# Optimization experiments

Measured on AMD Instinct MI355X. Metric: run time of the kernel, lower is better.

## Reference

```python
import jax, jax.numpy as jnp
import numpy as np

B, TAU, D, DX, DZ, H = 512, 4, 5, 256, 16, 64
M = D * DZ
COEFF_KL = 1.0
LOG2PI = float(np.log(2.0 * np.pi))


def setup_inputs() -> dict:
    ks = jax.random.split(jax.random.key(0), 12)
    s = 0.05
    return {
        "x": jax.random.normal(ks[0], (B, TAU, D, DX), jnp.float32),
        "y": jax.random.normal(ks[1], (B, D, DX), jnp.float32),
        "mask_param": jnp.full((TAU, M, M), 5.0, jnp.float32),
        "w_enc": ((0.9 * jax.random.uniform(ks[2], (D, DZ, DX)) + 0.1) / DX).astype(jnp.float32),
        "w_dec": ((0.9 * jax.random.uniform(ks[3], (D, DX, DZ)) + 0.1) / DZ).astype(jnp.float32),
        "enc_W0": jax.random.normal(ks[4], (DZ, DX, H), jnp.float32) * s,
        "enc_b0": jnp.zeros((DZ, H), jnp.float32),
        "enc_W1": jax.random.normal(ks[5], (DZ, H), jnp.float32) * s,
        "enc_b1": jnp.zeros((DZ,), jnp.float32),
        "dec_W0": jax.random.normal(ks[6], (DX, DZ, H), jnp.float32) * s,
        "dec_b0": jnp.zeros((DX, H), jnp.float32),
        "dec_W1": jax.random.normal(ks[7], (DX, H), jnp.float32) * s,
        "dec_b1": jnp.zeros((DX,), jnp.float32),
        "t_W0": jax.random.normal(ks[8], (M, TAU * M, H), jnp.float32) * s,
        "t_b0": jnp.zeros((M, H), jnp.float32),
        "t_W1": jax.random.normal(ks[9], (M, H), jnp.float32) * s,
        "t_b1": jnp.zeros((M,), jnp.float32),
        "logvar_enc": jnp.full((D,), -1.0, jnp.float32),
        "logvar_dec": jnp.full((D,), -1.0, jnp.float32),
        "t_logvar": jnp.full((D, DZ), -4.0, jnp.float32),
    }


def _encode(x, w_enc, W0, b0, W1, b1):
    # x: (..., D, DX) -> mu: (..., D, DZ); d_z tiny MLPs gated by mixing weights
    masked = w_enc * x[..., None, :]  # (..., D, DZ, DX)
    h = jax.nn.leaky_relu(jnp.einsum('...ijx,jxh->...ijh', masked, W0) + b0)
    return jnp.einsum('...ijh,jh->...ij', h, W1) + b1


def _forward(x, y, mask_param, w_enc, w_dec, enc_W0, enc_b0, enc_W1, enc_b1,
             dec_W0, dec_b0, dec_W1, dec_b1, t_W0, t_b0, t_W1, t_b1,
             logvar_enc, logvar_dec, t_logvar):
    b = x.shape[0]
    k_adj, k_ep, k_et = jax.random.split(jax.random.key(42), 3)
    # gumbel-sigmoid soft adjacency sample (temperature 1, drawhard=False)
    u = jax.random.uniform(k_adj, (b, TAU, M, M), minval=1e-6, maxval=1.0 - 1e-6)
    adj = jax.nn.sigmoid(mask_param + jnp.log(u) - jnp.log1p(-u))  # (b,TAU,M,M)
    # encoder q(z|x): reparameterized gaussian, per-feature logvar
    q_std = jnp.exp(0.5 * logvar_enc)[:, None]                     # (D,1)
    mu_past = _encode(x, w_enc, enc_W0, enc_b0, enc_W1, enc_b1)    # (b,TAU,D,DZ)
    z_past = mu_past + q_std * jax.random.normal(k_ep, mu_past.shape, jnp.float32)
    mu_t = _encode(y, w_enc, enc_W0, enc_b0, enc_W1, enc_b1)       # (b,D,DZ)
    z_t = mu_t + q_std * jax.random.normal(k_et, mu_t.shape, jnp.float32)
    # transition p(z_t|z_<t): per-node MLP on adjacency-gated past latents
    zp = z_past.reshape(b, TAU, M)
    gated = adj * zp[:, :, None, :]                                # (b,TAU,node,src)
    gated = gated.transpose(0, 2, 1, 3).reshape(b, M, TAU * M)
    ht = jax.nn.leaky_relu(jnp.einsum('bmi,mih->bmh', gated, t_W0) + t_b0)
    pz_mu = (jnp.einsum('bmh,mh->bm', ht, t_W1) + t_b1).reshape(b, D, DZ)
    pz_std = jnp.exp(0.5 * t_logvar)                               # (D,DZ)
    # decoder p(x|z): d_x tiny MLPs on mixing-mask-gated latents
    masked_z = w_dec * z_t[:, :, None, :]                          # (b,D,DX,DZ)
    hd = jax.nn.leaky_relu(jnp.einsum('bijz,jzh->bijh', masked_z, dec_W0) + dec_b0)
    px_mu = jnp.einsum('bijh,jh->bij', hd, dec_W1) + dec_b1        # (b,D,DX)
    px_std = jnp.exp(0.5 * logvar_dec)[:, None]                    # (D,1)
    # ELBO: gaussian recon log-lik + analytic gaussian KL(q || p_transition)
    recon = -0.5 * ((y - px_mu) / px_std) ** 2 - jnp.log(px_std) - 0.5 * LOG2PI
    recon = recon.sum(axis=(1, 2)).mean()
    kl = (jnp.log(pz_std) - 0.5 * logvar_enc[:, None]
          + (q_std ** 2 + (mu_t - pz_mu) ** 2) / (2.0 * pz_std ** 2) - 0.5)
    kl = kl.sum(axis=(1, 2)).mean()
    return -(recon - COEFF_KL * kl)


def reference(x, y, mask_param, w_enc, w_dec, enc_W0, enc_b0, enc_W1, enc_b1,
              dec_W0, dec_b0, dec_W1, dec_b1, t_W0, t_b0, t_W1, t_b1,
              logvar_enc, logvar_dec, t_logvar):
    return _forward(x, y, mask_param, w_enc, w_dec, enc_W0, enc_b0, enc_W1, enc_b1,
                    dec_W0, dec_b0, dec_W1, dec_b1, t_W0, t_b0, t_W1, t_b1,
                    logvar_enc, logvar_dec, t_logvar)
```

## Files before the change

kernel.cpp:

```cpp
#include <hip/hip_runtime.h>
#include <cstdint>

constexpr int NB = 512, NTAU = 4, ND = 5, NDX = 256, NDZ = 16, NH = 64;
constexpr int NM  = ND * NDZ;
constexpr int NTM = NTAU * NM;
constexpr int NSAMP = NB * NTAU + NB;
constexpr float LOG2PI_F = 1.8378770664093453f;

typedef __attribute__((ext_vector_type(8))) short bf16x8;
typedef __attribute__((ext_vector_type(4))) float f32x4;

__device__ __forceinline__ unsigned long long mix64(unsigned long long z) {
  z += 0x9E3779B97F4A7C15ull;
  z = (z ^ (z >> 30)) * 0xBF58476D1CE4E5B9ull;
  z = (z ^ (z >> 27)) * 0x94D049BB133111EBull;
  return z ^ (z >> 31);
}
__device__ __forceinline__ float u01f(unsigned long long h) {
  return ((float)(unsigned)(h >> 40) + 0.5f) * (1.0f / 16777216.0f);
}
__device__ __forceinline__ float rng_normal(unsigned long long salt, unsigned long long idx) {
  float u1 = u01f(mix64(salt + 2ull * idx));
  float u2 = u01f(mix64(salt + 2ull * idx + 1ull));
  float r = sqrtf(-2.0f * logf(u1));
  return r * cosf(6.283185307179586f * u2);
}
constexpr unsigned long long SALT_ADJ = 0x1000000000000ull;
constexpr unsigned long long SALT_EP  = 0x2000000000000ull;
constexpr unsigned long long SALT_ET  = 0x3000000000000ull;

__device__ __forceinline__ short f2bf(float f) {
  unsigned u = __float_as_uint(f);
  unsigned r = (u + 0x7FFFu + ((u >> 16) & 1u)) >> 16;
  return (short)r;
}

__global__ __launch_bounds__(256) void k_prepW(
    const float* __restrict__ x, const float* __restrict__ y, short* __restrict__ Abf,
    const float* __restrict__ w_enc, const float* __restrict__ eW0, short* __restrict__ PtE,
    const float* __restrict__ w_dec, const float* __restrict__ dW0, short* __restrict__ QtD,
    const float* __restrict__ mask_param, float* __restrict__ em,
    const float* __restrict__ tW0, short* __restrict__ TtB,
    float* __restrict__ yT)
{
  __shared__ short lds[64][65];
  const int bid = blockIdx.x;
  if (bid < 1600) {
    int e0 = (bid * 256 + threadIdx.x) * 8;
    int d = e0 / (NSAMP * NDX);
    int r = e0 % (NSAMP * NDX);
    int s = r >> 8, x0 = r & 255;
    const float* src = (s < NB * NTAU)
        ? &x[((size_t)s * ND + d) * NDX + x0]
        : &y[((size_t)(s - NB * NTAU) * ND + d) * NDX + x0];
    float4 f0 = *(const float4*)src;
    float4 f1 = *(const float4*)(src + 4);
    bf16x8 o;
    o[0] = f2bf(f0.x); o[1] = f2bf(f0.y); o[2] = f2bf(f0.z); o[3] = f2bf(f0.w);
    o[4] = f2bf(f1.x); o[5] = f2bf(f1.y); o[6] = f2bf(f1.z); o[7] = f2bf(f1.w);
    *(bf16x8*)&Abf[e0] = o;
  } else if (bid < 2240) {
    int e0 = ((bid - 1600) * 256 + threadIdx.x) * 8;
    int d = e0 / (1024 * NDX);
    int r = e0 % (1024 * NDX);
    int col = r >> 8, x0 = r & 255;
    int z = col >> 6, h = col & 63;
    const float* wep = &w_enc[((size_t)d * NDZ + z) * NDX + x0];
    float4 w0 = *(const float4*)wep;
    float4 w1 = *(const float4*)(wep + 4);
    const float* w0base = &eW0[((size_t)z * NDX + x0) * NH + h];
    bf16x8 o;
    o[0] = f2bf(w0.x * w0base[0 * NH]); o[1] = f2bf(w0.y * w0base[1 * NH]);
    o[2] = f2bf(w0.z * w0base[2 * NH]); o[3] = f2bf(w0.w * w0base[3 * NH]);
    o[4] = f2bf(w1.x * w0base[4 * NH]); o[5] = f2bf(w1.y * w0base[5 * NH]);
    o[6] = f2bf(w1.z * w0base[6 * NH]); o[7] = f2bf(w1.w * w0base[7 * NH]);
    *(bf16x8*)&PtE[e0] = o;
  } else if (bid < 2560) {
    int t = (bid - 2240) * 256 + threadIdx.x;
    int d = t / (NDX * NH);
    int r = t % (NDX * NH);
    int xx = r >> 6, h = r & 63;
    size_t base = (size_t)t * 32;
    #pragma unroll
    for (int z = 0; z < NDZ; ++z)
      QtD[base + z] = f2bf(w_dec[((size_t)d * NDX + xx) * NDZ + z] *
                           dW0[((size_t)xx * NDZ + z) * NH + h]);
    #pragma unroll
    for (int z = NDZ; z < 32; ++z) QtD[base + z] = 0;
  } else if (bid < 2660) {
    int idx = (bid - 2560) * 256 + threadIdx.x;
    em[idx] = expf(-mask_param[idx]);
  } else if (bid < 3060) {
    int r = bid - 2660;
    int kt = r % 5, m = r / 5;
    int k0 = kt * 64;
    for (int idx = threadIdx.x; idx < 64 * 64; idx += 256) {
      int hh = idx & 63, kk = idx >> 6;
      lds[kk][hh] = f2bf(tW0[((size_t)m * NTM + k0 + kk) * NH + hh]);
    }
    __syncthreads();
    for (int idx = threadIdx.x; idx < 64 * 64; idx += 256) {
      int kk = idx & 63, hh = idx >> 6;
      TtB[((size_t)m * NH + hh) * NTM + k0 + kk] = lds[kk][hh];
    }
  } else {
    int e0 = ((bid - 3060) * 256 + threadIdx.x) * 4;
    int d = e0 / (NDX * NB);
    int rem = e0 % (NDX * NB);
    int xx = rem >> 9, b0 = rem & 511;
    float4 o;
    o.x = y[((size_t)(b0 + 0) * ND + d) * NDX + xx];
    o.y = y[((size_t)(b0 + 1) * ND + d) * NDX + xx];
    o.z = y[((size_t)(b0 + 2) * ND + d) * NDX + xx];
    o.w = y[((size_t)(b0 + 3) * ND + d) * NDX + xx];
    *(float4*)&yT[e0] = o;
  }
}

__global__ __launch_bounds__(512) void k_enc_mfma(
    const short* __restrict__ Abf, const short* __restrict__ PtE,
    const float* __restrict__ b0, const float* __restrict__ W1,
    const float* __restrict__ b1, float* __restrict__ mu_all)
{
  __shared__ __align__(16) short Bs[64 * 264];

  const int d = blockIdx.z, zq = blockIdx.y;
  const int s0 = blockIdx.x * 128;
  const int tid = threadIdx.x;
  const int w = tid >> 6, l = tid & 63;
  const int lrow = l & 15, g = l >> 4;

  const short* Arow = Abf + ((size_t)(d * NSAMP + s0 + w * 16 + lrow)) * NDX + g * 8;
  bf16x8 a[8];
  #pragma unroll
  for (int ks = 0; ks < 8; ++ks) a[ks] = *(const bf16x8*)(Arow + ks * 32);

  const int stg_row = tid >> 3;
  const int stg_c   = (tid & 7) * 32;

  for (int zi = 0; zi < 4; ++zi) {
    const int z = zq * 4 + zi;
    {
      const short* src = PtE + ((size_t)(d * 1024 + z * 64 + stg_row)) * NDX + stg_c;
      short* dst = Bs + stg_row * 264 + stg_c;
      #pragma unroll
      for (int j = 0; j < 4; ++j)
        *(bf16x8*)(dst + j * 8) = *(const bf16x8*)(src + j * 8);
    }
    __syncthreads();

    f32x4 acc[4] = {};
    #pragma unroll
    for (int nt = 0; nt < 4; ++nt) {
      const short* Brow = Bs + (nt * 16 + lrow) * 264 + g * 8;
      #pragma unroll
      for (int ks = 0; ks < 8; ++ks) {
        bf16x8 bv = *(const bf16x8*)(Brow + ks * 32);
        acc[nt] = __builtin_amdgcn_mfma_f32_16x16x32_bf16(a[ks], bv, acc[nt], 0, 0, 0);
      }
    }

    float b0v[4], w1v[4];
    #pragma unroll
    for (int nt = 0; nt < 4; ++nt) {
      int h = nt * 16 + lrow;
      b0v[nt] = b0[z * NH + h];
      w1v[nt] = W1[z * NH + h];
    }
    const float b1v = b1[z];
    #pragma unroll
    for (int reg = 0; reg < 4; ++reg) {
      float v = 0.0f;
      #pragma unroll
      for (int nt = 0; nt < 4; ++nt) {
        float hv = acc[nt][reg] + b0v[nt];
        hv = fmaxf(hv, 0.01f * hv);
        v += hv * w1v[nt];
      }
      #pragma unroll
      for (int off = 1; off < 16; off <<= 1) v += __shfl_xor(v, off, 16);
      if (lrow == 0) {
        int s = s0 + w * 16 + g * 4 + reg;
        mu_all[(size_t)s * NM + d * NDZ + z] = v + b1v;
      }
    }
    __syncthreads();
  }
}

__global__ __launch_bounds__(256) void k_noise(
    const float* __restrict__ mu_all, const float* __restrict__ lve,
    float* __restrict__ z_past, float* __restrict__ mu_t, float* __restrict__ z_t)
{
  int i = blockIdx.x * 256 + threadIdx.x;
  int s = i / NM, m = i - s * NM;
  int d = m >> 4;
  float mu = mu_all[i];
  float qs = expf(0.5f * lve[d]);
  if (s < NB * NTAU) {
    float eps = rng_normal(SALT_EP, (unsigned long long)s * NM + m);
    z_past[i] = mu + qs * eps;
  } else {
    int b = s - NB * NTAU;
    float eps = rng_normal(SALT_ET, (unsigned long long)b * NM + m);
    size_t o = (size_t)b * NM + m;
    mu_t[o] = mu;
    z_t[o]  = mu + qs * eps;
  }
}

__global__ __launch_bounds__(512) void k_trans_mfma(
    const float* __restrict__ em, const float* __restrict__ z_past,
    const short* __restrict__ TtB,
    const float* __restrict__ tb0, const float* __restrict__ tW1,
    const float* __restrict__ tb1, const float* __restrict__ lve,
    const float* __restrict__ t_logvar, const float* __restrict__ mu_t,
    float* __restrict__ kl_partial)
{
  __shared__ __align__(16) short Bls[64 * 328];
  __shared__ float ems[NTM];
  __shared__ float klb[8];

  const int m = blockIdx.y;
  const int b0 = blockIdx.x * 128;
  const int tid = threadIdx.x;
  const int w = tid >> 6, l = tid & 63;
  const int lrow = l & 15, g = l >> 4;

  for (int i = tid; i < NTM; i += 512) {
    int t = i / NM, s = i - t * NM;
    ems[i] = em[(t * NM + m) * NM + s];
  }
  {
    const int r = tid >> 3;
    const int c0 = (tid & 7) * 40;
    const short* src = TtB + ((size_t)(m * NH + r)) * NTM + c0;
    short* dst = Bls + r * 328 + c0;
    #pragma unroll
    for (int j = 0; j < 5; ++j)
      *(bf16x8*)(dst + j * 8) = *(const bf16x8*)(src + j * 8);
  }
  __syncthreads();

  const int brow = b0 + w * 16 + lrow;
  const float* zrow = z_past + (size_t)brow * NTM;
  bf16x8 a[10];
  #pragma unroll
  for (int ks = 0; ks < 10; ++ks) {
    const int tm0 = g * 8 + ks * 32;
    const int t = tm0 / NM;
    const int s0 = tm0 - t * NM;
    unsigned long long aibase =
        ((unsigned long long)((brow * NTAU + t) * NM + m)) * NM + s0;
    unsigned long long h0 = mix64(SALT_ADJ + aibase);
    unsigned long long h1 = mix64(SALT_ADJ + aibase + 2);
    unsigned long long h2 = mix64(SALT_ADJ + aibase + 4);
    unsigned long long h3 = mix64(SALT_ADJ + aibase + 6);
    float u[8];
    u[0] = ((float)(unsigned)(h0 >> 40) + 0.5f) * (1.0f / 16777216.0f);
    u[1] = ((float)((unsigned)(h0 >> 16) & 0xFFFFFFu) + 0.5f) * (1.0f / 16777216.0f);
    u[2] = ((float)(unsigned)(h1 >> 40) + 0.5f) * (1.0f / 16777216.0f);
    u[3] = ((float)((unsigned)(h1 >> 16) & 0xFFFFFFu) + 0.5f) * (1.0f / 16777216.0f);
    u[4] = ((float)(unsigned)(h2 >> 40) + 0.5f) * (1.0f / 16777216.0f);
    u[5] = ((float)((unsigned)(h2 >> 16) & 0xFFFFFFu) + 0.5f) * (1.0f / 16777216.0f);
    u[6] = ((float)(unsigned)(h3 >> 40) + 0.5f) * (1.0f / 16777216.0f);
    u[7] = ((float)((unsigned)(h3 >> 16) & 0xFFFFFFu) + 0.5f) * (1.0f / 16777216.0f);
    float4 z0 = *(const float4*)(zrow + tm0);
    float4 z1 = *(const float4*)(zrow + tm0 + 4);
    const float* zvp0 = &z0.x;
    const float* zvp1 = &z1.x;
    #pragma unroll
    for (int j = 0; j < 8; ++j) {
      float uu = fminf(fmaxf(u[j], 1e-6f), 1.0f - 1e-6f);
      float e = ems[tm0 + j];
      float den = fmaf(e, 1.0f - uu, uu);
      float adj = uu * __builtin_amdgcn_rcpf(den);
      float zv = (j < 4) ? zvp0[j] : zvp1[j - 4];
      a[ks][j] = f2bf(adj * zv);
    }
  }

  f32x4 acc[4] = {};
  #pragma unroll
  for (int nt = 0; nt < 4; ++nt) {
    const short* Brow = Bls + (nt * 16 + lrow) * 328 + g * 8;
    #pragma unroll
    for (int ks = 0; ks < 10; ++ks) {
      bf16x8 bv = *(const bf16x8*)(Brow + ks * 32);
      acc[nt] = __builtin_amdgcn_mfma_f32_16x16x32_bf16(a[ks], bv, acc[nt], 0, 0, 0);
    }
  }

  float b0v[4], w1v[4];
  #pragma unroll
  for (int nt = 0; nt < 4; ++nt) {
    int h = nt * 16 + lrow;
    b0v[nt] = tb0[m * NH + h];
    w1v[nt] = tW1[m * NH + h];
  }

  const int d = m >> 4;
  const float lv_t = t_logvar[m];
  const float lv_e = lve[d];
  const float inv2var = 0.5f * expf(-lv_t);
  const float qvar = expf(lv_e);
  const float cterm = 0.5f * lv_t - 0.5f * lv_e - 0.5f;
  const float bv1 = tb1[m];

  float klw = 0.0f;
  #pragma unroll
  for (int reg = 0; reg < 4; ++reg) {
    float v = 0.0f;
    #pragma unroll
    for (int nt = 0; nt < 4; ++nt) {
      float hv = acc[nt][reg] + b0v[nt];
      hv = fmaxf(hv, 0.01f * hv);
      v += hv * w1v[nt];
    }
    #pragma unroll
    for (int off = 1; off < 16; off <<= 1) v += __shfl_xor(v, off, 16);
    if (lrow == 0) {
      int b = b0 + w * 16 + g * 4 + reg;
      float pz = v + bv1;
      float diff = mu_t[(size_t)b * NM + m] - pz;
      klw += cterm + (qvar + diff * diff) * inv2var;
    }
  }
  klw += __shfl_xor(klw, 16, 64);
  klw += __shfl_xor(klw, 32, 64);

  if (l == 0) klb[w] = klw;
  __syncthreads();
  if (tid == 0) {
    float s = 0.f;
    #pragma unroll
    for (int i = 0; i < 8; ++i) s += klb[i];
    kl_partial[blockIdx.x * NM + m] = s;
  }
}

__global__ __launch_bounds__(256) void k_dec_mfma(
    const float* __restrict__ zt, const short* __restrict__ QtD,
    const float* __restrict__ yT, const float* __restrict__ db0,
    const float* __restrict__ dW1, const float* __restrict__ db1,
    const float* __restrict__ lvd, float* __restrict__ rec_partial)
{
  const int d = blockIdx.z, xx = blockIdx.y, mb = blockIdx.x;
  const int w = threadIdx.x >> 6, l = threadIdx.x & 63;
  const int lrow = l & 15, g = l >> 4;

  bf16x8 bfr[4];
  const short* Bbase = QtD + ((size_t)((d * NDX + xx) * NH)) * 32;
  #pragma unroll
  for (int nt = 0; nt < 4; ++nt)
    bfr[nt] = *(const bf16x8*)(Bbase + (nt * 16 + lrow) * 32 + g * 8);

  f32x4 acc[4][4] = {};
  #pragma unroll
  for (int mt = 0; mt < 4; ++mt) {
    int b = mb * 256 + w * 64 + mt * 16 + lrow;
    bf16x8 a = {0, 0, 0, 0, 0, 0, 0, 0};
    if (g < 2) {
      const float* zp = zt + (size_t)b * NM + d * NDZ + g * 8;
      float4 f0 = *(const float4*)zp;
      float4 f1 = *(const float4*)(zp + 4);
      a[0] = f2bf(f0.x); a[1] = f2bf(f0.y); a[2] = f2bf(f0.z); a[3] = f2bf(f0.w);
      a[4] = f2bf(f1.x); a[5] = f2bf(f1.y); a[6] = f2bf(f1.z); a[7] = f2bf(f1.w);
    }
    #pragma unroll
    for (int nt = 0; nt < 4; ++nt)
      acc[mt][nt] = __builtin_amdgcn_mfma_f32_16x16x32_bf16(a, bfr[nt], acc[mt][nt], 0, 0, 0);
  }

  float db0v[4], dW1v[4];
  #pragma unroll
  for (int nt = 0; nt < 4; ++nt) {
    int h = nt * 16 + lrow;
    db0v[nt] = db0[xx * NH + h];
    dW1v[nt] = dW1[xx * NH + h];
  }
  const float lv = lvd[d];
  const float inv_std = expf(-0.5f * lv);
  const float cterm = -0.5f * lv - 0.5f * LOG2PI_F;
  const float b1v = db1[xx];

  float racc = 0.0f;
  #pragma unroll
  for (int mt = 0; mt < 4; ++mt) {
    float rs[4];
    #pragma unroll
    for (int reg = 0; reg < 4; ++reg) {
      float v = 0.0f;
      #pragma unroll
      for (int nt = 0; nt < 4; ++nt) {
        float hv = acc[mt][nt][reg] + db0v[nt];
        hv = fmaxf(hv, 0.01f * hv);
        v += hv * dW1v[nt];
      }
      #pragma unroll
      for (int off = 1; off < 16; off <<= 1) v += __shfl_xor(v, off, 16);
      rs[reg] = v;
    }
    if (lrow == 0) {
      int b = mb * 256 + w * 64 + mt * 16 + g * 4;
      float4 yv = *(const float4*)&yT[((size_t)d * NDX + xx) * NB + b];
      const float* yvp = &yv.x;
      #pragma unroll
      for (int reg = 0; reg < 4; ++reg) {
        float px = rs[reg] + b1v;
        float e = (yvp[reg] - px) * inv_std;
        racc += -0.5f * e * e + cterm;
      }
    }
  }
  racc += __shfl_xor(racc, 16, 64);
  racc += __shfl_xor(racc, 32, 64);

  __shared__ float rb[4];
  if (l == 0) rb[w] = racc;
  __syncthreads();
  if (threadIdx.x == 0)
    rec_partial[((size_t)d * NDX + xx) * 2 + mb] = rb[0] + rb[1] + rb[2] + rb[3];
}

__global__ __launch_bounds__(256) void k_reduce(
    const float* __restrict__ rp, const float* __restrict__ kp,
    float* __restrict__ out)
{
  __shared__ float sr[4], sk[4];
  float r = 0.f, k = 0.f;
  for (int i = threadIdx.x; i < 2560; i += 256) r += rp[i];
  for (int i = threadIdx.x; i < 320; i += 256) k += kp[i];
  #pragma unroll
  for (int off = 32; off; off >>= 1) {
    r += __shfl_xor(r, off, 64);
    k += __shfl_xor(k, off, 64);
  }
  int wv = threadIdx.x >> 6;
  if ((threadIdx.x & 63) == 0) { sr[wv] = r; sk[wv] = k; }
  __syncthreads();
  if (threadIdx.x == 0) {
    float R = sr[0] + sr[1] + sr[2] + sr[3];
    float K = sk[0] + sk[1] + sk[2] + sk[3];
    out[0] = (K - R) / (float)NB;
  }
}

extern "C" void kernel_launch(void* const* d_in, const int* in_sizes, int n_in,
                              void* d_out, int out_size, void* d_ws, size_t ws_size,
                              hipStream_t stream) {
  (void)in_sizes; (void)n_in; (void)out_size; (void)ws_size;
  const float* x        = (const float*)d_in[0];
  const float* y        = (const float*)d_in[1];
  const float* mask_p   = (const float*)d_in[2];
  const float* w_enc    = (const float*)d_in[3];
  const float* w_dec    = (const float*)d_in[4];
  const float* enc_W0   = (const float*)d_in[5];
  const float* enc_b0   = (const float*)d_in[6];
  const float* enc_W1   = (const float*)d_in[7];
  const float* enc_b1   = (const float*)d_in[8];
  const float* dec_W0   = (const float*)d_in[9];
  const float* dec_b0   = (const float*)d_in[10];
  const float* dec_W1   = (const float*)d_in[11];
  const float* dec_b1   = (const float*)d_in[12];
  const float* t_W0     = (const float*)d_in[13];
  const float* t_b0     = (const float*)d_in[14];
  const float* t_W1     = (const float*)d_in[15];
  const float* t_b1     = (const float*)d_in[16];
  const float* lv_enc   = (const float*)d_in[17];
  const float* lv_dec   = (const float*)d_in[18];
  const float* t_logvar = (const float*)d_in[19];

  float* ws     = (float*)d_ws;
  float* z_past = ws;
  float* mu_t   = z_past + 163840;
  float* z_t    = mu_t + 40960;
  float* rec_p  = z_t + 40960;
  float* kl_p   = rec_p + 2560;
  float* em     = kl_p + 320;
  float* mu_all = em + 25600;
  float* yTb    = mu_all + 204800;
  short* Abf    = (short*)(yTb + 655360);
  short* PtE    = Abf + 5 * NSAMP * NDX;
  short* QtD    = PtE + 5 * 1024 * NDX;
  short* TtB    = QtD + 5 * NDX * NH * 32;

  k_prepW<<<3700, 256, 0, stream>>>(
      x, y, Abf, w_enc, enc_W0, PtE, w_dec, dec_W0, QtD, mask_p, em, t_W0, TtB, yTb);

  k_enc_mfma<<<dim3(NSAMP / 128, 4, ND), 512, 0, stream>>>(
      Abf, PtE, enc_b0, enc_W1, enc_b1, mu_all);
  k_noise<<<NSAMP * NM / 256, 256, 0, stream>>>(mu_all, lv_enc, z_past, mu_t, z_t);
  k_trans_mfma<<<dim3(NB / 128, NM), 512, 0, stream>>>(
      em, z_past, TtB, t_b0, t_W1, t_b1, lv_enc, t_logvar, mu_t, kl_p);
  k_dec_mfma<<<dim3(2, NDX, ND), 256, 0, stream>>>(
      z_t, QtD, yTb, dec_b0, dec_W1, dec_b1, lv_dec, rec_p);
  k_reduce<<<1, 256, 0, stream>>>(rec_p, kl_p, (float*)d_out);
}
```

Baseline: 80.08 us.

## Fuse bf16 input conversion and noise into encoder, merge transition and decoder kernels

```diff
diff --git a/kernel.cpp b/kernel.cpp
--- a/kernel.cpp
+++ b/kernel.cpp
@@ -36,7 +36,7 @@
 }
 
 __global__ __launch_bounds__(256) void k_prepW(
-    const float* __restrict__ x, const float* __restrict__ y, short* __restrict__ Abf,
+    const float* __restrict__ y,
     const float* __restrict__ w_enc, const float* __restrict__ eW0, short* __restrict__ PtE,
     const float* __restrict__ w_dec, const float* __restrict__ dW0, short* __restrict__ QtD,
     const float* __restrict__ mask_param, float* __restrict__ em,
@@ -45,22 +45,8 @@
 {
   __shared__ short lds[64][65];
   const int bid = blockIdx.x;
-  if (bid < 1600) {
+  if (bid < 640) {
     int e0 = (bid * 256 + threadIdx.x) * 8;
-    int d = e0 / (NSAMP * NDX);
-    int r = e0 % (NSAMP * NDX);
-    int s = r >> 8, x0 = r & 255;
-    const float* src = (s < NB * NTAU)
-        ? &x[((size_t)s * ND + d) * NDX + x0]
-        : &y[((size_t)(s - NB * NTAU) * ND + d) * NDX + x0];
-    float4 f0 = *(const float4*)src;
-    float4 f1 = *(const float4*)(src + 4);
-    bf16x8 o;
-    o[0] = f2bf(f0.x); o[1] = f2bf(f0.y); o[2] = f2bf(f0.z); o[3] = f2bf(f0.w);
-    o[4] = f2bf(f1.x); o[5] = f2bf(f1.y); o[6] = f2bf(f1.z); o[7] = f2bf(f1.w);
-    *(bf16x8*)&Abf[e0] = o;
-  } else if (bid < 2240) {
-    int e0 = ((bid - 1600) * 256 + threadIdx.x) * 8;
     int d = e0 / (1024 * NDX);
     int r = e0 % (1024 * NDX);
     int col = r >> 8, x0 = r & 255;
@@ -75,8 +61,8 @@
     o[4] = f2bf(w1.x * w0base[4 * NH]); o[5] = f2bf(w1.y * w0base[5 * NH]);
     o[6] = f2bf(w1.z * w0base[6 * NH]); o[7] = f2bf(w1.w * w0base[7 * NH]);
     *(bf16x8*)&PtE[e0] = o;
-  } else if (bid < 2560) {
-    int t = (bid - 2240) * 256 + threadIdx.x;
+  } else if (bid < 960) {
+    int t = (bid - 640) * 256 + threadIdx.x;
     int d = t / (NDX * NH);
     int r = t % (NDX * NH);
     int xx = r >> 6, h = r & 63;
@@ -87,11 +73,11 @@
                            dW0[((size_t)xx * NDZ + z) * NH + h]);
     #pragma unroll
     for (int z = NDZ; z < 32; ++z) QtD[base + z] = 0;
-  } else if (bid < 2660) {
-    int idx = (bid - 2560) * 256 + threadIdx.x;
+  } else if (bid < 1060) {
+    int idx = (bid - 960) * 256 + threadIdx.x;
     em[idx] = expf(-mask_param[idx]);
-  } else if (bid < 3060) {
-    int r = bid - 2660;
+  } else if (bid < 1460) {
+    int r = bid - 1060;
     int kt = r % 5, m = r / 5;
     int k0 = kt * 64;
     for (int idx = threadIdx.x; idx < 64 * 64; idx += 256) {
@@ -104,7 +90,7 @@
       TtB[((size_t)m * NH + hh) * NTM + k0 + kk] = lds[kk][hh];
     }
   } else {
-    int e0 = ((bid - 3060) * 256 + threadIdx.x) * 4;
+    int e0 = ((bid - 1460) * 256 + threadIdx.x) * 4;
     int d = e0 / (NDX * NB);
     int rem = e0 % (NDX * NB);
     int xx = rem >> 9, b0 = rem & 511;
@@ -118,11 +104,14 @@
 }
 
 __global__ __launch_bounds__(512) void k_enc_mfma(
-    const short* __restrict__ Abf, const short* __restrict__ PtE,
+    const float* __restrict__ x, const float* __restrict__ y,
+    const short* __restrict__ PtE,
     const float* __restrict__ b0, const float* __restrict__ W1,
-    const float* __restrict__ b1, float* __restrict__ mu_all)
+    const float* __restrict__ b1, const float* __restrict__ lve,
+    float* __restrict__ z_past, float* __restrict__ mu_t, float* __restrict__ z_t)
 {
   __shared__ __align__(16) short Bs[64 * 264];
+  __shared__ float mu_s[128][4];
 
   const int d = blockIdx.z, zq = blockIdx.y;
   const int s0 = blockIdx.x * 128;
@@ -130,10 +119,21 @@
   const int w = tid >> 6, l = tid & 63;
   const int lrow = l & 15, g = l >> 4;
 
-  const short* Arow = Abf + ((size_t)(d * NSAMP + s0 + w * 16 + lrow)) * NDX + g * 8;
+  const int srow = s0 + w * 16 + lrow;
+  const float* Asrc = (srow < NB * NTAU)
+      ? &x[((size_t)srow * ND + d) * NDX]
+      : &y[((size_t)(srow - NB * NTAU) * ND + d) * NDX];
   bf16x8 a[8];
   #pragma unroll
-  for (int ks = 0; ks < 8; ++ks) a[ks] = *(const bf16x8*)(Arow + ks * 32);
+  for (int ks = 0; ks < 8; ++ks) {
+    const float* p = Asrc + g * 8 + ks * 32;
+    float4 f0 = *(const float4*)p;
+    float4 f1 = *(const float4*)(p + 4);
+    a[ks][0] = f2bf(f0.x); a[ks][1] = f2bf(f0.y);
+    a[ks][2] = f2bf(f0.z); a[ks][3] = f2bf(f0.w);
+    a[ks][4] = f2bf(f1.x); a[ks][5] = f2bf(f1.y);
+    a[ks][6] = f2bf(f1.z); a[ks][7] = f2bf(f1.w);
+  }
 
   const int stg_row = tid >> 3;
   const int stg_c   = (tid & 7) * 32;
@@ -179,248 +179,250 @@
       }
       #pragma unroll
       for (int off = 1; off < 16; off <<= 1) v += __shfl_xor(v, off, 16);
-      if (lrow == 0) {
-        int s = s0 + w * 16 + g * 4 + reg;
-        mu_all[(size_t)s * NM + d * NDZ + z] = v + b1v;
-      }
-    }
-    __syncthreads();
-  }
-}
-
-__global__ __launch_bounds__(256) void k_noise(
-    const float* __restrict__ mu_all, const float* __restrict__ lve,
-    float* __restrict__ z_past, float* __restrict__ mu_t, float* __restrict__ z_t)
-{
-  int i = blockIdx.x * 256 + threadIdx.x;
-  int s = i / NM, m = i - s * NM;
-  int d = m >> 4;
-  float mu = mu_all[i];
-  float qs = expf(0.5f * lve[d]);
-  if (s < NB * NTAU) {
-    float eps = rng_normal(SALT_EP, (unsigned long long)s * NM + m);
-    z_past[i] = mu + qs * eps;
-  } else {
-    int b = s - NB * NTAU;
-    float eps = rng_normal(SALT_ET, (unsigned long long)b * NM + m);
-    size_t o = (size_t)b * NM + m;
-    mu_t[o] = mu;
-    z_t[o]  = mu + qs * eps;
-  }
-}
-
-__global__ __launch_bounds__(512) void k_trans_mfma(
+      if (lrow == 0)
+        mu_s[w * 16 + g * 4 + reg][zi] = v + b1v;
+    }
+    __syncthreads();
+  }
+
+  {
+    const int sl = tid >> 2, zi = tid & 3;
+    const int z = zq * 4 + zi;
+    const int s = s0 + sl;
+    const int m = d * NDZ + z;
+    float mu = mu_s[sl][zi];
+    float qs = expf(0.5f * lve[d]);
+    if (s < NB * NTAU) {
+      float eps = rng_normal(SALT_EP, (unsigned long long)s * NM + m);
+      z_past[(size_t)s * NM + m] = mu + qs * eps;
+    } else {
+      int b = s - NB * NTAU;
+      float eps = rng_normal(SALT_ET, (unsigned long long)b * NM + m);
+      size_t o = (size_t)b * NM + m;
+      mu_t[o] = mu;
+      z_t[o]  = mu + qs * eps;
+    }
+  }
+}
+
+__global__ __launch_bounds__(512) void k_tail(
     const float* __restrict__ em, const float* __restrict__ z_past,
     const short* __restrict__ TtB,
     const float* __restrict__ tb0, const float* __restrict__ tW1,
     const float* __restrict__ tb1, const float* __restrict__ lve,
     const float* __restrict__ t_logvar, const float* __restrict__ mu_t,
-    float* __restrict__ kl_partial)
-{
-  __shared__ __align__(16) short Bls[64 * 328];
-  __shared__ float ems[NTM];
-  __shared__ float klb[8];
-
-  const int m = blockIdx.y;
-  const int b0 = blockIdx.x * 128;
-  const int tid = threadIdx.x;
-  const int w = tid >> 6, l = tid & 63;
-  const int lrow = l & 15, g = l >> 4;
-
-  for (int i = tid; i < NTM; i += 512) {
-    int t = i / NM, s = i - t * NM;
-    ems[i] = em[(t * NM + m) * NM + s];
-  }
-  {
-    const int r = tid >> 3;
-    const int c0 = (tid & 7) * 40;
-    const short* src = TtB + ((size_t)(m * NH + r)) * NTM + c0;
-    short* dst = Bls + r * 328 + c0;
-    #pragma unroll
-    for (int j = 0; j < 5; ++j)
-      *(bf16x8*)(dst + j * 8) = *(const bf16x8*)(src + j * 8);
-  }
-  __syncthreads();
-
-  const int brow = b0 + w * 16 + lrow;
-  const float* zrow = z_past + (size_t)brow * NTM;
-  bf16x8 a[10];
-  #pragma unroll
-  for (int ks = 0; ks < 10; ++ks) {
-    const int tm0 = g * 8 + ks * 32;
-    const int t = tm0 / NM;
-    const int s0 = tm0 - t * NM;
-    unsigned long long aibase =
-        ((unsigned long long)((brow * NTAU + t) * NM + m)) * NM + s0;
-    unsigned long long h0 = mix64(SALT_ADJ + aibase);
-    unsigned long long h1 = mix64(SALT_ADJ + aibase + 2);
-    unsigned long long h2 = mix64(SALT_ADJ + aibase + 4);
-    unsigned long long h3 = mix64(SALT_ADJ + aibase + 6);
-    float u[8];
-    u[0] = ((float)(unsigned)(h0 >> 40) + 0.5f) * (1.0f / 16777216.0f);
-    u[1] = ((float)((unsigned)(h0 >> 16) & 0xFFFFFFu) + 0.5f) * (1.0f / 16777216.0f);
-    u[2] = ((float)(unsigned)(h1 >> 40) + 0.5f) * (1.0f / 16777216.0f);
-    u[3] = ((float)((unsigned)(h1 >> 16) & 0xFFFFFFu) + 0.5f) * (1.0f / 16777216.0f);
-    u[4] = ((float)(unsigned)(h2 >> 40) + 0.5f) * (1.0f / 16777216.0f);
-    u[5] = ((float)((unsigned)(h2 >> 16) & 0xFFFFFFu) + 0.5f) * (1.0f / 16777216.0f);
-    u[6] = ((float)(unsigned)(h3 >> 40) + 0.5f) * (1.0f / 16777216.0f);
-    u[7] = ((float)((unsigned)(h3 >> 16) & 0xFFFFFFu) + 0.5f) * (1.0f / 16777216.0f);
-    float4 z0 = *(const float4*)(zrow + tm0);
-    float4 z1 = *(const float4*)(zrow + tm0 + 4);
-    const float* zvp0 = &z0.x;
-    const float* zvp1 = &z1.x;
-    #pragma unroll
-    for (int j = 0; j < 8; ++j) {
-      float uu = fminf(fmaxf(u[j], 1e-6f), 1.0f - 1e-6f);
-      float e = ems[tm0 + j];
-      float den = fmaf(e, 1.0f - uu, uu);
-      float adj = uu * __builtin_amdgcn_rcpf(den);
-      float zv = (j < 4) ? zvp0[j] : zvp1[j - 4];
-      a[ks][j] = f2bf(adj * zv);
-    }
-  }
-
-  f32x4 acc[4] = {};
-  #pragma unroll
-  for (int nt = 0; nt < 4; ++nt) {
-    const short* Brow = Bls + (nt * 16 + lrow) * 328 + g * 8;
-    #pragma unroll
-    for (int ks = 0; ks < 10; ++ks) {
-      bf16x8 bv = *(const bf16x8*)(Brow + ks * 32);
-      acc[nt] = __builtin_amdgcn_mfma_f32_16x16x32_bf16(a[ks], bv, acc[nt], 0, 0, 0);
-    }
-  }
-
-  float b0v[4], w1v[4];
-  #pragma unroll
-  for (int nt = 0; nt < 4; ++nt) {
-    int h = nt * 16 + lrow;
-    b0v[nt] = tb0[m * NH + h];
-    w1v[nt] = tW1[m * NH + h];
-  }
-
-  const int d = m >> 4;
-  const float lv_t = t_logvar[m];
-  const float lv_e = lve[d];
-  const float inv2var = 0.5f * expf(-lv_t);
-  const float qvar = expf(lv_e);
-  const float cterm = 0.5f * lv_t - 0.5f * lv_e - 0.5f;
-  const float bv1 = tb1[m];
-
-  float klw = 0.0f;
-  #pragma unroll
-  for (int reg = 0; reg < 4; ++reg) {
-    float v = 0.0f;
-    #pragma unroll
-    for (int nt = 0; nt < 4; ++nt) {
-      float hv = acc[nt][reg] + b0v[nt];
-      hv = fmaxf(hv, 0.01f * hv);
-      v += hv * w1v[nt];
-    }
-    #pragma unroll
-    for (int off = 1; off < 16; off <<= 1) v += __shfl_xor(v, off, 16);
-    if (lrow == 0) {
-      int b = b0 + w * 16 + g * 4 + reg;
-      float pz = v + bv1;
-      float diff = mu_t[(size_t)b * NM + m] - pz;
-      klw += cterm + (qvar + diff * diff) * inv2var;
-    }
-  }
-  klw += __shfl_xor(klw, 16, 64);
-  klw += __shfl_xor(klw, 32, 64);
-
-  if (l == 0) klb[w] = klw;
-  __syncthreads();
-  if (tid == 0) {
-    float s = 0.f;
-    #pragma unroll
-    for (int i = 0; i < 8; ++i) s += klb[i];
-    kl_partial[blockIdx.x * NM + m] = s;
-  }
-}
-
-__global__ __launch_bounds__(256) void k_dec_mfma(
+    float* __restrict__ kl_partial,
     const float* __restrict__ zt, const short* __restrict__ QtD,
     const float* __restrict__ yT, const float* __restrict__ db0,
     const float* __restrict__ dW1, const float* __restrict__ db1,
     const float* __restrict__ lvd, float* __restrict__ rec_partial)
 {
-  const int d = blockIdx.z, xx = blockIdx.y, mb = blockIdx.x;
-  const int w = threadIdx.x >> 6, l = threadIdx.x & 63;
-  const int lrow = l & 15, g = l >> 4;
-
-  bf16x8 bfr[4];
-  const short* Bbase = QtD + ((size_t)((d * NDX + xx) * NH)) * 32;
-  #pragma unroll
-  for (int nt = 0; nt < 4; ++nt)
-    bfr[nt] = *(const bf16x8*)(Bbase + (nt * 16 + lrow) * 32 + g * 8);
-
-  f32x4 acc[4][4] = {};
-  #pragma unroll
-  for (int mt = 0; mt < 4; ++mt) {
-    int b = mb * 256 + w * 64 + mt * 16 + lrow;
-    bf16x8 a = {0, 0, 0, 0, 0, 0, 0, 0};
-    if (g < 2) {
-      const float* zp = zt + (size_t)b * NM + d * NDZ + g * 8;
-      float4 f0 = *(const float4*)zp;
-      float4 f1 = *(const float4*)(zp + 4);
-      a[0] = f2bf(f0.x); a[1] = f2bf(f0.y); a[2] = f2bf(f0.z); a[3] = f2bf(f0.w);
-      a[4] = f2bf(f1.x); a[5] = f2bf(f1.y); a[6] = f2bf(f1.z); a[7] = f2bf(f1.w);
-    }
-    #pragma unroll
-    for (int nt = 0; nt < 4; ++nt)
-      acc[mt][nt] = __builtin_amdgcn_mfma_f32_16x16x32_bf16(a, bfr[nt], acc[mt][nt], 0, 0, 0);
-  }
-
-  float db0v[4], dW1v[4];
-  #pragma unroll
-  for (int nt = 0; nt < 4; ++nt) {
-    int h = nt * 16 + lrow;
-    db0v[nt] = db0[xx * NH + h];
-    dW1v[nt] = dW1[xx * NH + h];
-  }
-  const float lv = lvd[d];
-  const float inv_std = expf(-0.5f * lv);
-  const float cterm = -0.5f * lv - 0.5f * LOG2PI_F;
-  const float b1v = db1[xx];
-
-  float racc = 0.0f;
-  #pragma unroll
-  for (int mt = 0; mt < 4; ++mt) {
-    float rs[4];
+  __shared__ __align__(16) short Bls[64 * 328];
+  __shared__ float ems[NTM];
+  __shared__ float redb[8];
+
+  const int bid = blockIdx.x;
+  const int tid = threadIdx.x;
+
+  if (bid < 320) {
+    const int m = bid >> 2;
+    const int b0 = (bid & 3) * 128;
+    const int w = tid >> 6, l = tid & 63;
+    const int lrow = l & 15, g = l >> 4;
+
+    for (int i = tid; i < NTM; i += 512) {
+      int t = i / NM, s = i - t * NM;
+      ems[i] = em[(t * NM + m) * NM + s];
+    }
+    {
+      const int r = tid >> 3;
+      const int c0 = (tid & 7) * 40;
+      const short* src = TtB + ((size_t)(m * NH + r)) * NTM + c0;
+      short* dst = Bls + r * 328 + c0;
+      #pragma unroll
+      for (int j = 0; j < 5; ++j)
+        *(bf16x8*)(dst + j * 8) = *(const bf16x8*)(src + j * 8);
+    }
+    __syncthreads();
+
+    const int brow = b0 + w * 16 + lrow;
+    const float* zrow = z_past + (size_t)brow * NTM;
+    bf16x8 a[10];
+    #pragma unroll
+    for (int ks = 0; ks < 10; ++ks) {
+      const int tm0 = g * 8 + ks * 32;
+      const int t = tm0 / NM;
+      const int s0 = tm0 - t * NM;
+      unsigned long long aibase =
+          ((unsigned long long)((brow * NTAU + t) * NM + m)) * NM + s0;
+      unsigned long long h0 = mix64(SALT_ADJ + aibase);
+      unsigned long long h1 = mix64(SALT_ADJ + aibase + 2);
+      unsigned long long h2 = mix64(SALT_ADJ + aibase + 4);
+      unsigned long long h3 = mix64(SALT_ADJ + aibase + 6);
+      float u[8];
+      u[0] = ((float)(unsigned)(h0 >> 40) + 0.5f) * (1.0f / 16777216.0f);
+      u[1] = ((float)((unsigned)(h0 >> 16) & 0xFFFFFFu) + 0.5f) * (1.0f / 16777216.0f);
+      u[2] = ((float)(unsigned)(h1 >> 40) + 0.5f) * (1.0f / 16777216.0f);
+      u[3] = ((float)((unsigned)(h1 >> 16) & 0xFFFFFFu) + 0.5f) * (1.0f / 16777216.0f);
+      u[4] = ((float)(unsigned)(h2 >> 40) + 0.5f) * (1.0f / 16777216.0f);
+      u[5] = ((float)((unsigned)(h2 >> 16) & 0xFFFFFFu) + 0.5f) * (1.0f / 16777216.0f);
+      u[6] = ((float)(unsigned)(h3 >> 40) + 0.5f) * (1.0f / 16777216.0f);
+      u[7] = ((float)((unsigned)(h3 >> 16) & 0xFFFFFFu) + 0.5f) * (1.0f / 16777216.0f);
+      float4 z0 = *(const float4*)(zrow + tm0);
+      float4 z1 = *(const float4*)(zrow + tm0 + 4);
+      const float* zvp0 = &z0.x;
+      const float* zvp1 = &z1.x;
+      #pragma unroll
+      for (int j = 0; j < 8; ++j) {
+        float uu = fminf(fmaxf(u[j], 1e-6f), 1.0f - 1e-6f);
+        float e = ems[tm0 + j];
+        float den = fmaf(e, 1.0f - uu, uu);
+        float adj = uu * __builtin_amdgcn_rcpf(den);
+        float zv = (j < 4) ? zvp0[j] : zvp1[j - 4];
+        a[ks][j] = f2bf(adj * zv);
+      }
+    }
+
+    f32x4 acc[4] = {};
+    #pragma unroll
+    for (int nt = 0; nt < 4; ++nt) {
+      const short* Brow = Bls + (nt * 16 + lrow) * 328 + g * 8;
+      #pragma unroll
+      for (int ks = 0; ks < 10; ++ks) {
+        bf16x8 bv = *(const bf16x8*)(Brow + ks * 32);
+        acc[nt] = __builtin_amdgcn_mfma_f32_16x16x32_bf16(a[ks], bv, acc[nt], 0, 0, 0);
+      }
+    }
+
+    float b0v[4], w1v[4];
+    #pragma unroll
+    for (int nt = 0; nt < 4; ++nt) {
+      int h = nt * 16 + lrow;
+      b0v[nt] = tb0[m * NH + h];
+      w1v[nt] = tW1[m * NH + h];
+    }
+
+    const int d = m >> 4;
+    const float lv_t = t_logvar[m];
+    const float lv_e = lve[d];
+    const float inv2var = 0.5f * expf(-lv_t);
+    const float qvar = expf(lv_e);
+    const float cterm = 0.5f * lv_t - 0.5f * lv_e - 0.5f;
+    const float bv1 = tb1[m];
+
+    float klw = 0.0f;
     #pragma unroll
     for (int reg = 0; reg < 4; ++reg) {
       float v = 0.0f;
       #pragma unroll
       for (int nt = 0; nt < 4; ++nt) {
-        float hv = acc[mt][nt][reg] + db0v[nt];
+        float hv = acc[nt][reg] + b0v[nt];
         hv = fmaxf(hv, 0.01f * hv);
-        v += hv * dW1v[nt];
+        v += hv * w1v[nt];
       }
       #pragma unroll
       for (int off = 1; off < 16; off <<= 1) v += __shfl_xor(v, off, 16);
-      rs[reg] = v;
-    }
-    if (lrow == 0) {
-      int b = mb * 256 + w * 64 + mt * 16 + g * 4;
-      float4 yv = *(const float4*)&yT[((size_t)d * NDX + xx) * NB + b];
-      const float* yvp = &yv.x;
+      if (lrow == 0) {
+        int b = b0 + w * 16 + g * 4 + reg;
+        float pz = v + bv1;
+        float diff = mu_t[(size_t)b * NM + m] - pz;
+        klw += cterm + (qvar + diff * diff) * inv2var;
+      }
+    }
+    klw += __shfl_xor(klw, 16, 64);
+    klw += __shfl_xor(klw, 32, 64);
+
+    if (l == 0) redb[w] = klw;
+    __syncthreads();
+    if (tid == 0) {
+      float s = 0.f;
+      #pragma unroll
+      for (int i = 0; i < 8; ++i) s += redb[i];
+      kl_partial[(bid & 3) * NM + m] = s;
+    }
+  } else {
+    const int idx = bid - 320;
+    const int d = idx >> 8, xx = idx & 255;
+    const int w8 = tid >> 6, l = tid & 63;
+    const int mb = w8 >> 2, w = w8 & 3;
+    const int lrow = l & 15, g = l >> 4;
+
+    bf16x8 bfr[4];
+    const short* Bbase = QtD + ((size_t)((d * NDX + xx) * NH)) * 32;
+    #pragma unroll
+    for (int nt = 0; nt < 4; ++nt)
+      bfr[nt] = *(const bf16x8*)(Bbase + (nt * 16 + lrow) * 32 + g * 8);
+
+    f32x4 acc[4][4] = {};
+    #pragma unroll
+    for (int mt = 0; mt < 4; ++mt) {
+      int b = mb * 256 + w * 64 + mt * 16 + lrow;
+      bf16x8 a = {0, 0, 0, 0, 0, 0, 0, 0};
+      if (g < 2) {
+        const float* zp = zt + (size_t)b * NM + d * NDZ + g * 8;
+        float4 f0 = *(const float4*)zp;
+        float4 f1 = *(const float4*)(zp + 4);
+        a[0] = f2bf(f0.x); a[1] = f2bf(f0.y); a[2] = f2bf(f0.z); a[3] = f2bf(f0.w);
+        a[4] = f2bf(f1.x); a[5] = f2bf(f1.y); a[6] = f2bf(f1.z); a[7] = f2bf(f1.w);
+      }
+      #pragma unroll
+      for (int nt = 0; nt < 4; ++nt)
+        acc[mt][nt] = __builtin_amdgcn_mfma_f32_16x16x32_bf16(a, bfr[nt], acc[mt][nt], 0, 0, 0);
+    }
+
+    float db0v[4], dW1v[4];
+    #pragma unroll
+    for (int nt = 0; nt < 4; ++nt) {
+      int h = nt * 16 + lrow;
+      db0v[nt] = db0[xx * NH + h];
+      dW1v[nt] = dW1[xx * NH + h];
+    }
+    const float lv = lvd[d];
+    const float inv_std = expf(-0.5f * lv);
+    const float cterm = -0.5f * lv - 0.5f * LOG2PI_F;
+    const float b1v = db1[xx];
+
+    float racc = 0.0f;
+    #pragma unroll
+    for (int mt = 0; mt < 4; ++mt) {
+      float rs[4];
       #pragma unroll
       for (int reg = 0; reg < 4; ++reg) {
-        float px = rs[reg] + b1v;
-        float e = (yvp[reg] - px) * inv_std;
-        racc += -0.5f * e * e + cterm;
-      }
-    }
-  }
-  racc += __shfl_xor(racc, 16, 64);
-  racc += __shfl_xor(racc, 32, 64);
-
-  __shared__ float rb[4];
-  if (l == 0) rb[w] = racc;
-  __syncthreads();
-  if (threadIdx.x == 0)
-    rec_partial[((size_t)d * NDX + xx) * 2 + mb] = rb[0] + rb[1] + rb[2] + rb[3];
+        float v = 0.0f;
+        #pragma unroll
+        for (int nt = 0; nt < 4; ++nt) {
+          float hv = acc[mt][nt][reg] + db0v[nt];
+          hv = fmaxf(hv, 0.01f * hv);
+          v += hv * dW1v[nt];
+        }
+        #pragma unroll
+        for (int off = 1; off < 16; off <<= 1) v += __shfl_xor(v, off, 16);
+        rs[reg] = v;
+      }
+      if (lrow == 0) {
+        int b = mb * 256 + w * 64 + mt * 16 + g * 4;
+        float4 yv = *(const float4*)&yT[((size_t)d * NDX + xx) * NB + b];
+        const float* yvp = &yv.x;
+        #pragma unroll
+        for (int reg = 0; reg < 4; ++reg) {
+          float px = rs[reg] + b1v;
+          float e = (yvp[reg] - px) * inv_std;
+          racc += -0.5f * e * e + cterm;
+        }
+      }
+    }
+    racc += __shfl_xor(racc, 16, 64);
+    racc += __shfl_xor(racc, 32, 64);
+
+    if (l == 0) redb[w8] = racc;
+    __syncthreads();
+    if (tid == 0) {
+      float s = 0.f;
+      #pragma unroll
+      for (int i = 0; i < 8; ++i) s += redb[i];
+      rec_partial[(size_t)d * NDX + xx] = s;
+    }
+  }
 }
 
 __global__ __launch_bounds__(256) void k_reduce(
@@ -429,7 +431,7 @@
 {
   __shared__ float sr[4], sk[4];
   float r = 0.f, k = 0.f;
-  for (int i = threadIdx.x; i < 2560; i += 256) r += rp[i];
+  for (int i = threadIdx.x; i < 1280; i += 256) r += rp[i];
   for (int i = threadIdx.x; i < 320; i += 256) k += kp[i];
   #pragma unroll
   for (int off = 32; off; off >>= 1) {
@@ -476,24 +478,20 @@
   float* mu_t   = z_past + 163840;
   float* z_t    = mu_t + 40960;
   float* rec_p  = z_t + 40960;
-  float* kl_p   = rec_p + 2560;
+  float* kl_p   = rec_p + 1280;
   float* em     = kl_p + 320;
-  float* mu_all = em + 25600;
-  float* yTb    = mu_all + 204800;
-  short* Abf    = (short*)(yTb + 655360);
-  short* PtE    = Abf + 5 * NSAMP * NDX;
+  float* yTb    = em + 25600;
+  short* PtE    = (short*)(yTb + 655360);
   short* QtD    = PtE + 5 * 1024 * NDX;
   short* TtB    = QtD + 5 * NDX * NH * 32;
 
-  k_prepW<<<3700, 256, 0, stream>>>(
-      x, y, Abf, w_enc, enc_W0, PtE, w_dec, dec_W0, QtD, mask_p, em, t_W0, TtB, yTb);
+  k_prepW<<<2100, 256, 0, stream>>>(
+      y, w_enc, enc_W0, PtE, w_dec, dec_W0, QtD, mask_p, em, t_W0, TtB, yTb);
 
   k_enc_mfma<<<dim3(NSAMP / 128, 4, ND), 512, 0, stream>>>(
-      Abf, PtE, enc_b0, enc_W1, enc_b1, mu_all);
-  k_noise<<<NSAMP * NM / 256, 256, 0, stream>>>(mu_all, lv_enc, z_past, mu_t, z_t);
-  k_trans_mfma<<<dim3(NB / 128, NM), 512, 0, stream>>>(
-      em, z_past, TtB, t_b0, t_W1, t_b1, lv_enc, t_logvar, mu_t, kl_p);
-  k_dec_mfma<<<dim3(2, NDX, ND), 256, 0, stream>>>(
+      x, y, PtE, enc_b0, enc_W1, enc_b1, lv_enc, z_past, mu_t, z_t);
+  k_tail<<<1600, 512, 0, stream>>>(
+      em, z_past, TtB, t_b0, t_W1, t_b1, lv_enc, t_logvar, mu_t, kl_p,
       z_t, QtD, yTb, dec_b0, dec_W1, dec_b1, lv_dec, rec_p);
   k_reduce<<<1, 256, 0, stream>>>(rec_p, kl_p, (float*)d_out);
 }
```

Result: faster. 72.44 us (-9.5%).
